# Performance work log

Hardware: AMD Instinct MI355X
Metric: run time of the kernel (lower is better)

## Reference

```python
import jax, jax.numpy as jnp
import numpy as np

B, NW, NS, SL = 32, 500, 50, 40
EMB, HID, VOCAB, E = 300, 150, 50000, 563200
N = B * (NW + NS)
MAXPOS = 512


def _sinusoid(n_pos, d):
    pos = np.arange(n_pos)[:, None].astype(np.float64)
    i = np.arange(d)[None, :]
    ang = pos / np.power(10000.0, 2 * (i // 2) / d)
    tab = np.zeros((n_pos, d))
    tab[:, 0::2] = np.sin(ang[:, 0::2])
    tab[:, 1::2] = np.cos(ang[:, 1::2])
    tab[0] = 0.0  # padding_idx=0
    return jnp.asarray(tab, dtype=jnp.float32)

_POS_TAB = _sinusoid(MAXPOS + 1, EMB)


def setup_inputs():
    keys = iter(jax.random.split(jax.random.key(0), 48))
    def nrm(shape, s=0.05):
        return jax.random.normal(next(keys), shape, dtype=jnp.float32) * s
    inp = {}
    inp["x"] = jax.random.randint(next(keys), (B, NW), 0, VOCAB, dtype=jnp.int32)
    inp["sent_x"] = jax.random.randint(next(keys), (B, NS, SL), 0, VOCAB, dtype=jnp.int32)
    inp["edge_index"] = jax.random.randint(next(keys), (2, E), 0, N, dtype=jnp.int32)
    inp["embed_table"] = nrm((VOCAB, EMB)).at[0].set(0.0)  # padding_idx=0
    for h in range(2, 8):
        inp["conv_w%d" % h] = nrm((50, 1, h, EMB))
        inp["conv_b%d" % h] = nrm((50,))
    inp["cnn_proj_w"] = nrm((HID, EMB)); inp["cnn_proj_b"] = nrm((HID,))
    inp["lstm_w_ih_l0"] = nrm((2, 4 * HID, HID)); inp["lstm_w_hh_l0"] = nrm((2, 4 * HID, HID))
    inp["lstm_b_ih_l0"] = nrm((2, 4 * HID)); inp["lstm_b_hh_l0"] = nrm((2, 4 * HID))
    inp["lstm_w_ih_l1"] = nrm((2, 4 * HID, 2 * HID)); inp["lstm_w_hh_l1"] = nrm((2, 4 * HID, HID))
    inp["lstm_b_ih_l1"] = nrm((2, 4 * HID)); inp["lstm_b_hh_l1"] = nrm((2, 4 * HID))
    inp["lstm_proj_w"] = nrm((HID, 2 * HID)); inp["lstm_proj_b"] = nrm((HID,))
    inp["gc0_w"] = nrm((HID, EMB)); inp["gc0_b"] = nrm((HID,))
    inp["gc1_w"] = nrm((HID, HID)); inp["gc1_b"] = nrm((HID,))
    inp["gc2_w"] = nrm((HID, HID)); inp["gc2_b"] = nrm((HID,))
    return inp


def _forward(x, sent_x, edge_index, embed_table, conv_ws, conv_bs,
             cnn_proj_w, cnn_proj_b, w_ih0, w_hh0, b_ih0, b_hh0,
             w_ih1, w_hh1, b_ih1, b_hh1, lstm_proj_w, lstm_proj_b,
             gc0_w, gc0_b, gc1_w, gc1_b, gc2_w, gc2_b):
    Bsz, S, L = sent_x.shape
    Nn = Bsz * S
    emb_words = embed_table[x]                                   # [B, NW, EMB]
    tok = embed_table[sent_x].reshape(Nn, L, EMB)                # [Nn, L, EMB]
    sentlen = (sent_x != 0).sum(-1).reshape(Nn)                  # token count per sentence
    a = jnp.arange(L)
    input_pos = jnp.where(a[None, :] < sentlen[:, None], a[None, :] + 1, 0)
    enc = tok + _POS_TAB[input_pos]
    # CNN ngram features: conv heights 2..7, full-width kernels == windowed matmuls
    feats = []
    for w, b in zip(conv_ws, conv_bs):
        h = w.shape[2]
        acc = b + sum(jnp.einsum('nld,od->nlo', enc[:, k:L - h + 1 + k, :], w[:, 0, k, :]) for k in range(h))
        feats.append(jnp.max(jax.nn.relu(acc), axis=1))          # [Nn, 50]
    ngram = jnp.concatenate(feats, axis=1)                        # [Nn, 300]
    snode_pos = jnp.tile(jnp.arange(S), Bsz)
    cnn_feat = ((ngram + _POS_TAB[snode_pos]) @ cnn_proj_w.T + cnn_proj_b).reshape(Bsz, S, HID)
    glen = (sent_x[:, :, 0] != 0).sum(-1)                         # valid sentence count per graph

    def lstm_dir(xs, w_ih, w_hh, bias):
        def step(carry, xt):
            hh, cc = carry
            g = xt @ w_ih.T + hh @ w_hh.T + bias
            i, f, gg, o = jnp.split(g, 4, axis=-1)
            cc = jax.nn.sigmoid(f) * cc + jax.nn.sigmoid(i) * jnp.tanh(gg)
            hh = jax.nn.sigmoid(o) * jnp.tanh(cc)
            return (hh, cc), hh
        z = jnp.zeros((xs.shape[0], HID), xs.dtype)
        _, hs = jax.lax.scan(step, (z, z), jnp.swapaxes(xs, 0, 1))
        return jnp.swapaxes(hs, 0, 1)

    def rev_within(xs):
        # reverse only the first glen[b] steps (packed-sequence semantics)
        T = xs.shape[1]; t = jnp.arange(T)
        idx = jnp.where(t[None, :] < glen[:, None], glen[:, None] - 1 - t[None, :], t[None, :])
        return jnp.take_along_axis(xs, idx[:, :, None], axis=1)

    def bidir(xs, w_ih, w_hh, b_i, b_h):
        f = lstm_dir(xs, w_ih[0], w_hh[0], b_i[0] + b_h[0])
        r = rev_within(lstm_dir(rev_within(xs), w_ih[1], w_hh[1], b_i[1] + b_h[1]))
        return jnp.concatenate([f, r], axis=-1)

    h1 = bidir(cnn_feat, w_ih0, w_hh0, b_ih0, b_hh0)
    h2 = bidir(h1, w_ih1, w_hh1, b_ih1, b_hh1)
    mask = (jnp.arange(S)[None, :] < glen[:, None]).astype(h2.dtype)[:, :, None]
    lstm_feat = (h2 * mask) @ lstm_proj_w.T + lstm_proj_b
    sent_out = jnp.concatenate([cnn_feat, lstm_feat], axis=-1)    # [B, S, 300]
    nodes = jnp.concatenate([emb_words, sent_out], axis=1)        # [B, NW+S, 300]
    nodes = (nodes @ gc0_w.T + gc0_b).reshape(-1, HID)            # [N, 150]
    Nt = nodes.shape[0]
    loop = jnp.arange(Nt, dtype=edge_index.dtype)
    src = jnp.concatenate([edge_index[0], loop])                  # add self-loops
    dst = jnp.concatenate([edge_index[1], loop])
    deg = jax.ops.segment_sum(jnp.ones(src.shape[0], nodes.dtype), dst, num_segments=Nt)
    dis = jnp.where(deg > 0, jax.lax.rsqrt(deg), 0.0)
    norm = (dis[src] * dis[dst])[:, None]

    def gcn(xin, w, bias):
        xw = xin @ w.T
        return jax.ops.segment_sum(xw[src] * norm, dst, num_segments=Nt) + bias

    h = jax.nn.elu(gcn(nodes, gc1_w, gc1_b))
    # F.dropout with training=False -> identity
    return gcn(h, gc2_w, gc2_b), emb_words


def reference(x, sent_x, edge_index, embed_table, conv_w2, conv_b2, conv_w3, conv_b3,
              conv_w4, conv_b4, conv_w5, conv_b5, conv_w6, conv_b6, conv_w7, conv_b7,
              cnn_proj_w, cnn_proj_b, lstm_w_ih_l0, lstm_w_hh_l0, lstm_b_ih_l0, lstm_b_hh_l0,
              lstm_w_ih_l1, lstm_w_hh_l1, lstm_b_ih_l1, lstm_b_hh_l1, lstm_proj_w, lstm_proj_b,
              gc0_w, gc0_b, gc1_w, gc1_b, gc2_w, gc2_b):
    conv_ws = [conv_w2, conv_w3, conv_w4, conv_w5, conv_w6, conv_w7]
    conv_bs = [conv_b2, conv_b3, conv_b4, conv_b5, conv_b6, conv_b7]
    return _forward(x, sent_x, edge_index, embed_table, conv_ws, conv_bs,
                    cnn_proj_w, cnn_proj_b, lstm_w_ih_l0, lstm_w_hh_l0, lstm_b_ih_l0, lstm_b_hh_l0,
                    lstm_w_ih_l1, lstm_w_hh_l1, lstm_b_ih_l1, lstm_b_hh_l1, lstm_proj_w, lstm_proj_b,
                    gc0_w, gc0_b, gc1_w, gc1_b, gc2_w, gc2_b)
```

## Files before the change

### kernel.cpp

```cpp
#include <hip/hip_runtime.h>
#include <stdint.h>
#include <math.h>

#define EDGES 563200
#define NNODES 17600
#define OUT0SZ 2640000
#define MROWS 64000
#define MPAD  64016
#define KSTRIDE 2112

typedef _Float16 h2 __attribute__((ext_vector_type(2)));
typedef _Float16 h4 __attribute__((ext_vector_type(4)));
typedef _Float16 v8h __attribute__((ext_vector_type(8)));
typedef float v4f __attribute__((ext_vector_type(4)));

__device__ __forceinline__ float sigm(float x){ return 1.f / (1.f + expf(-x)); }

__device__ __forceinline__ float fdot2_(h2 a, h2 b, float c){
#if __has_builtin(__builtin_amdgcn_fdot2)
  return __builtin_amdgcn_fdot2(a, b, c, false);
#else
  return c + (float)a.x * (float)b.x + (float)a.y * (float)b.y;
#endif
}

__device__ __forceinline__ void stage16(const char* g, char* lds_base, int lane){
#if __has_builtin(__builtin_amdgcn_global_load_lds)
  __builtin_amdgcn_global_load_lds(
      (const __attribute__((address_space(1))) void*)g,
      (__attribute__((address_space(3))) void*)lds_base, 16, 0, 0);
#else
  uint4 v = *(const uint4*)g;
  *(uint4*)(lds_base + lane * 16) = v;
#endif
}

__global__ void gcnk_postab(float* __restrict__ pos){
  int idx = blockIdx.x * 256 + threadIdx.x;
  if (idx >= 513 * 300) return;
  int p = idx / 300, i = idx - p * 300;
  float v = 0.f;
  if (p != 0){
    double expo = (double)(2 * (i / 2)) / 300.0;
    double ang = (double)p / pow(10000.0, expo);
    v = (float)((i & 1) ? cos(ang) : sin(ang));
  }
  pos[idx] = v;
}

__global__ void gcnk_prep(const int* __restrict__ sx, int* __restrict__ sentlen,
                          int* __restrict__ glen){
  int tid = blockIdx.x * 256 + threadIdx.x;
  if (tid < 1600){
    int c = 0;
    for (int j = 0; j < 40; j++) c += (sx[tid * 40 + j] != 0);
    sentlen[tid] = c;
  } else if (tid < 1632){
    int b = tid - 1600, c = 0;
    for (int s = 0; s < 50; s++) c += (sx[b * 2000 + s * 40] != 0);
    glen[b] = c;
  }
}

__global__ void gcnk_rowmap(const int* __restrict__ glen, int* __restrict__ rowmap){
  int i = blockIdx.x * 256 + threadIdx.x;
  if (i >= 1600) return;
  int b = i / 50, t = i - b * 50, g = glen[b];
  rowmap[i] = b * 50 + ((t < g) ? (g - 1 - t) : t);
}

__global__ void gcnk_embw(const int* __restrict__ x, const float* __restrict__ tab,
                          float4* __restrict__ out){
  int idx = blockIdx.x * 256 + threadIdx.x;
  if (idx >= 16000 * 75) return;
  int row = idx / 75, q = idx - row * 75;
  const float4* t = (const float4*)tab;
  out[idx] = t[x[row] * 75 + q];
}

__global__ void gcnk_zeroi(unsigned int* __restrict__ p, int n){
  int i = blockIdx.x * 256 + threadIdx.x;
  if (i < n) p[i] = 0u;
}

__global__ void gcnk_ench(const int* __restrict__ sx, const float* __restrict__ tab,
                          const float* __restrict__ pos, const int* __restrict__ sentlen,
                          _Float16* __restrict__ ench){
  int idx = blockIdx.x * 256 + threadIdx.x;
  if (idx >= MPAD * 75) return;
  int row = idx / 75, q = idx - row * 75;
  int d = q * 4;
  h4 o; o[0] = (_Float16)0.f; o[1] = (_Float16)0.f; o[2] = (_Float16)0.f; o[3] = (_Float16)0.f;
  if (row < MROWS){
    int n = row / 40, l = row - n * 40;
    int tok = sx[n * 40 + l];
    int p = (l < sentlen[n]) ? (l + 1) : 0;
    float4 a = *(const float4*)(tab + (size_t)tok * 300 + d);
    float4 b = *(const float4*)(pos + (size_t)p * 300 + d);
    o[0] = (_Float16)(a.x + b.x); o[1] = (_Float16)(a.y + b.y);
    o[2] = (_Float16)(a.z + b.z); o[3] = (_Float16)(a.w + b.w);
  }
  *(h4*)(ench + (size_t)row * 300 + d) = o;
}

__global__ void gcnk_bpack(const float* w2, const float* w3, const float* w4,
                           const float* w5, const float* w6, const float* w7,
                           const float* c2, const float* c3, const float* c4,
                           const float* c5, const float* c6, const float* c7,
                           _Float16* __restrict__ Bp, float* __restrict__ bias_p){
  int idx = blockIdx.x * 256 + threadIdx.x;
  if (idx < 2 * 160 * KSTRIDE){
    int n = idx / KSTRIDE, kk = idx - n * KSTRIDE;
    int g = n / 160, c = n - g * 160;
    _Float16 v = (_Float16)0.f;
    if (c < 150){
      int H = 3 * g + 2 + c / 50, o = c % 50;
      if (kk < 300 * H){
        const float* w;
        switch (H){ case 2: w = w2; break; case 3: w = w3; break;
                    case 4: w = w4; break; case 5: w = w5; break;
                    case 6: w = w6; break; default: w = w7; break; }
        v = (_Float16)w[o * 300 * H + kk];
      }
    }
    Bp[idx] = v;
  }
  if (idx < 320){
    int g = idx / 160, c = idx - g * 160;
    float bv = 0.f;
    if (c < 150){
      int H = 3 * g + 2 + c / 50, o = c % 50;
      const float* cbp;
      switch (H){ case 2: cbp = c2; break; case 3: cbp = c3; break;
                  case 4: cbp = c4; break; case 5: cbp = c5; break;
                  case 6: cbp = c6; break; default: cbp = c7; break; }
      bv = cbp[o];
    }
    bias_p[idx] = bv;
  }
}

__global__ __launch_bounds__(256)
void gcnk_convmfma(const _Float16* __restrict__ A, const _Float16* __restrict__ Bp,
                   const float* __restrict__ bias_p, unsigned int* __restrict__ ngram_u){
  __shared__ __align__(1024) char smem[36864];
  _Float16* Asm = (_Float16*)smem;
  _Float16* Bsm = (_Float16*)(smem + 16384);
  float* Cs = (float*)smem;
  const int tid = threadIdx.x;
  const int m0 = blockIdx.x * 128;
  const int grp = blockIdx.y;
  const char* Abase = (const char*)A;
  const char* Bbase = (const char*)(Bp + (size_t)grp * 160 * KSTRIDE);
  const int kmax = grp ? 2112 : 1216;
  const int w = tid >> 6, lane = tid & 63;
  const int wm = (w >> 1) * 64, wn = (w & 1) * 80;
  const int fm = lane & 15, fq = lane >> 4;
  const int lrow = lane >> 3;
  const int loff = (((lane & 7) ^ lrow) << 4);

  v4f acc[4][5] = {};

  for (int kc = 0; kc < kmax; kc += 64){
    #pragma unroll
    for (int ii = 0; ii < 4; ii++){
      int i = w * 4 + ii;
      const char* g = Abase + (size_t)(m0 + i * 8 + lrow) * 600 + kc * 2 + loff;
      stage16(g, (char*)Asm + i * 1024, lane);
    }
    #pragma unroll
    for (int jj = 0; jj < 5; jj++){
      int j = w * 5 + jj;
      const char* g = Bbase + (size_t)(j * 8 + lrow) * (KSTRIDE * 2) + kc * 2 + loff;
      stage16(g, (char*)Bsm + j * 1024, lane);
    }
    __syncthreads();
    #pragma unroll
    for (int ks = 0; ks < 2; ks++){
      const int axor = (ks * 64 + fq * 16) ^ ((fm & 7) << 4);
      v8h af[4], bf[5];
      #pragma unroll
      for (int mt = 0; mt < 4; mt++)
        af[mt] = *(const v8h*)((const char*)Asm + (wm + mt * 16 + fm) * 128 + axor);
      #pragma unroll
      for (int nt = 0; nt < 5; nt++)
        bf[nt] = *(const v8h*)((const char*)Bsm + (wn + nt * 16 + fm) * 128 + axor);
      #pragma unroll
      for (int mt = 0; mt < 4; mt++)
        #pragma unroll
        for (int nt = 0; nt < 5; nt++)
          acc[mt][nt] = __builtin_amdgcn_mfma_f32_16x16x32_f16(af[mt], bf[nt], acc[mt][nt], 0, 0, 0);
    }
    __syncthreads();
  }

  for (int p = 0; p < 5; p++){
    __syncthreads();
    #pragma unroll
    for (int nt = 0; nt < 5; nt++){
      int cstart = wn + nt * 16;
      if ((cstart >> 5) == p){
        int co = cstart - p * 32 + fm;
        #pragma unroll
        for (int mt = 0; mt < 4; mt++)
          #pragma unroll
          for (int r = 0; r < 4; r++)
            Cs[(wm + mt * 16 + fq * 4 + r) * 33 + co] = acc[mt][nt][r];
      }
    }
    __syncthreads();
    if (tid < 128){
      int cl = tid & 31, si = tid >> 5;
      int col = p * 32 + cl;
      if (col < 150){
        int H = 3 * grp + 2 + col / 50, lh = 41 - H;
        int sent = m0 / 40 + si;
        if (sent < 1600){
          int rlo = sent * 40; if (rlo < m0) rlo = m0;
          int rhi = sent * 40 + lh; if (rhi > m0 + 128) rhi = m0 + 128;
          if (rlo < rhi){
            float bv = bias_p[grp * 160 + col];
            float vmax = 0.f;
            for (int r = rlo; r < rhi; r++){
              float v = Cs[(r - m0) * 33 + cl] + bv;
              vmax = fmaxf(vmax, v);
            }
            atomicMax(ngram_u + sent * 300 + grp * 150 + col, __float_as_uint(vmax));
          }
        }
      }
    }
  }
}

__global__ void gcnk_addpos(float* __restrict__ ngram, const float* __restrict__ pos){
  int idx = blockIdx.x * 256 + threadIdx.x;
  if (idx >= 1600 * 300) return;
  int row = idx / 300, d = idx - row * 300;
  ngram[idx] += pos[(row % 50) * 300 + d];
}

template<int BM, int BN, int WMT, int WNT, int OUTH>
__global__ __launch_bounds__(256)
void gcnk_mgemm(const float* __restrict__ A, const float* __restrict__ Wt,
                const float* __restrict__ b1, const float* __restrict__ b2,
                void* __restrict__ Cv, int M, int N, int K){
  __shared__ __align__(16) _Float16 As[BM * 40];
  __shared__ __align__(16) _Float16 Bs[BN * 40];
  const int tid = threadIdx.x;
  const int m0 = blockIdx.x * BM, n0 = blockIdx.y * BN;
  const int w = tid >> 6, lane = tid & 63;
  const int wm = (w >> 1) * (WMT * 16), wn = (w & 1) * (WNT * 16);
  const int fm = lane & 15, fq = lane >> 4;
  v4f acc[WMT][WNT] = {};
  const int nch = (K + 31) >> 5;
  for (int ch = 0; ch < nch; ch++){
    int kc = ch * 32;
    #pragma unroll
    for (int j = 0; j < BM / 64; j++){
      int u = tid + 256 * j;
      int row = u >> 2, cb = (u & 3) * 8;
      int gm = m0 + row, gk = kc + cb;
      v8h vv;
      if (gm < M && gk + 8 <= K){
        const float* p = A + (size_t)gm * K + gk;
        #pragma unroll
        for (int e = 0; e < 8; e++) vv[e] = (_Float16)p[e];
      } else {
        #pragma unroll
        for (int e = 0; e < 8; e++)
          vv[e] = (gm < M && gk + e < K) ? (_Float16)A[(size_t)gm * K + gk + e] : (_Float16)0.f;
      }
      *(v8h*)(As + row * 40 + cb) = vv;
    }
    {
      int row = tid >> 2, cb = (tid & 3) * 8;
      int gn = n0 + row, gk = kc + cb;
      v8h vv;
      if (gn < N && gk + 8 <= K){
        const float* p = Wt + (size_t)gn * K + gk;
        #pragma unroll
        for (int e = 0; e < 8; e++) vv[e] = (_Float16)p[e];
      } else {
        #pragma unroll
        for (int e = 0; e < 8; e++)
          vv[e] = (gn < N && gk + e < K) ? (_Float16)Wt[(size_t)gn * K + gk + e] : (_Float16)0.f;
      }
      *(v8h*)(Bs + row * 40 + cb) = vv;
    }
    __syncthreads();
    v8h af[WMT], bf[WNT];
    #pragma unroll
    for (int mt = 0; mt < WMT; mt++)
      af[mt] = *(const v8h*)(As + (wm + mt * 16 + fm) * 40 + fq * 8);
    #pragma unroll
    for (int nt = 0; nt < WNT; nt++)
      bf[nt] = *(const v8h*)(Bs + (wn + nt * 16 + fm) * 40 + fq * 8);
    #pragma unroll
    for (int mt = 0; mt < WMT; mt++)
      #pragma unroll
      for (int nt = 0; nt < WNT; nt++)
        acc[mt][nt] = __builtin_amdgcn_mfma_f32_16x16x32_f16(af[mt], bf[nt], acc[mt][nt], 0, 0, 0);
    __syncthreads();
  }
  #pragma unroll
  for (int nt = 0; nt < WNT; nt++){
    int gn = n0 + wn + nt * 16 + fm;
    if (gn >= N) continue;
    float badd = (b1 ? b1[gn] : 0.f) + (b2 ? b2[gn] : 0.f);
    #pragma unroll
    for (int mt = 0; mt < WMT; mt++)
      #pragma unroll
      for (int r = 0; r < 4; r++){
        int gm = m0 + wm + mt * 16 + fq * 4 + r;
        if (gm < M){
          float val = acc[mt][nt][r] + badd;
          if (OUTH) ((_Float16*)Cv)[(size_t)gm * 160 + gn] = (_Float16)val;
          else      ((float*)Cv)[(size_t)gm * N + gn] = val;
        }
      }
  }
}

__global__ __launch_bounds__(256)
void gcnk_mgemmF(const float* __restrict__ A1, const int* __restrict__ mapA,
                 const float* __restrict__ A2, const int* __restrict__ mapB,
                 const int* __restrict__ glen, int usemask,
                 const float* __restrict__ Wt, const float* __restrict__ b1,
                 const float* __restrict__ b2, float* __restrict__ C,
                 int M, int N, int K){
  const int BM = 64, WMT = 2, WNT = 2;
  __shared__ __align__(16) _Float16 As[BM * 40];
  __shared__ __align__(16) _Float16 Bs[64 * 40];
  const int tid = threadIdx.x;
  const int m0 = blockIdx.x * BM, n0 = blockIdx.y * 64;
  const int w = tid >> 6, lane = tid & 63;
  const int wm = (w >> 1) * (WMT * 16), wn = (w & 1) * (WNT * 16);
  const int fm = lane & 15, fq = lane >> 4;
  v4f acc[WMT][WNT] = {};
  const int nch = (K + 31) >> 5;
  for (int ch = 0; ch < nch; ch++){
    int kc = ch * 32;
    {
      int row = tid >> 2, cb = (tid & 3) * 8;
      int gm = m0 + row, gk = kc + cb;
      v8h vv;
      bool ok = (gm < M);
      if (ok && usemask){
        int b = gm / 50;
        if (gm - b * 50 >= glen[b]) ok = false;
      }
      if (!ok){
        #pragma unroll
        for (int e = 0; e < 8; e++) vv[e] = (_Float16)0.f;
      } else if (!A2){
        int r = mapA ? mapA[gm] : gm;
        const float* base = A1 + (size_t)r * K;
        if (gk + 8 <= K){
          #pragma unroll
          for (int e = 0; e < 8; e++) vv[e] = (_Float16)base[gk + e];
        } else {
          #pragma unroll
          for (int e = 0; e < 8; e++)
            vv[e] = (gk + e < K) ? (_Float16)base[gk + e] : (_Float16)0.f;
        }
      } else {
        int rA = mapA ? mapA[gm] : gm;
        int rB = mapB ? mapB[gm] : gm;
        const float* pa = A1 + (size_t)rA * 150;
        const float* pb = A2 + (size_t)rB * 150;
        if (gk + 8 <= 150){
          #pragma unroll
          for (int e = 0; e < 8; e++) vv[e] = (_Float16)pa[gk + e];
        } else if (gk >= 150){
          #pragma unroll
          for (int e = 0; e < 8; e++)
            vv[e] = (gk + e < K) ? (_Float16)pb[gk + e - 150] : (_Float16)0.f;
        } else {
          #pragma unroll
          for (int e = 0; e < 8; e++){
            int c = gk + e;
            vv[e] = (c < 150) ? (_Float16)pa[c]
                  : ((c < K) ? (_Float16)pb[c - 150] : (_Float16)0.f);
          }
        }
      }
      *(v8h*)(As + row * 40 + cb) = vv;
    }
    {
      int row = tid >> 2, cb = (tid & 3) * 8;
      int gn = n0 + row, gk = kc + cb;
      v8h vv;
      if (gn < N && gk + 8 <= K){
        const float* p = Wt + (size_t)gn * K + gk;
        #pragma unroll
        for (int e = 0; e < 8; e++) vv[e] = (_Float16)p[e];
      } else {
        #pragma unroll
        for (int e = 0; e < 8; e++)
          vv[e] = (gn < N && gk + e < K) ? (_Float16)Wt[(size_t)gn * K + gk + e] : (_Float16)0.f;
      }
      *(v8h*)(Bs + row * 40 + cb) = vv;
    }
    __syncthreads();
    v8h af[WMT], bf[WNT];
    #pragma unroll
    for (int mt = 0; mt < WMT; mt++)
      af[mt] = *(const v8h*)(As + (wm + mt * 16 + fm) * 40 + fq * 8);
    #pragma unroll
    for (int nt = 0; nt < WNT; nt++)
      bf[nt] = *(const v8h*)(Bs + (wn + nt * 16 + fm) * 40 + fq * 8);
    #pragma unroll
    for (int mt = 0; mt < WMT; mt++)
      #pragma unroll
      for (int nt = 0; nt < WNT; nt++)
        acc[mt][nt] = __builtin_amdgcn_mfma_f32_16x16x32_f16(af[mt], bf[nt], acc[mt][nt], 0, 0, 0);
    __syncthreads();
  }
  #pragma unroll
  for (int nt = 0; nt < WNT; nt++){
    int gn = n0 + wn + nt * 16 + fm;
    if (gn >= N) continue;
    float badd = (b1 ? b1[gn] : 0.f) + (b2 ? b2[gn] : 0.f);
    #pragma unroll
    for (int mt = 0; mt < WMT; mt++)
      #pragma unroll
      for (int r = 0; r < 4; r++){
        int gm = m0 + wm + mt * 16 + fq * 4 + r;
        if (gm < M) C[(size_t)gm * N + gn] = acc[mt][nt][r] + badd;
      }
  }
}

__global__ __launch_bounds__(256)
void gcnk_mgemmN(const int* __restrict__ x, const float* __restrict__ tab,
                 const float* __restrict__ cnnf, const float* __restrict__ lstmf,
                 const float* __restrict__ Wt, const float* __restrict__ b1,
                 float* __restrict__ C, int N){
  const int M = NNODES, K = 300;
  __shared__ __align__(16) _Float16 As[128 * 40];
  __shared__ __align__(16) _Float16 Bs[64 * 40];
  const int tid = threadIdx.x;
  const int m0 = blockIdx.x * 128, n0 = blockIdx.y * 64;
  const int w = tid >> 6, lane = tid & 63;
  const int wm = (w >> 1) * 64, wn = (w & 1) * 32;
  const int fm = lane & 15, fq = lane >> 4;
  v4f acc[4][2] = {};
  for (int ch = 0; ch < 10; ch++){
    int kc = ch * 32;
    #pragma unroll
    for (int j = 0; j < 2; j++){
      int u = tid + 256 * j;
      int row = u >> 2, cb = (u & 3) * 8;
      int gm = m0 + row, gk = kc + cb;
      v8h vv;
      if (gm < M){
        int b = gm / 550, jj = gm - b * 550;
        if (jj < 500){
          const float* p = tab + (size_t)x[b * 500 + jj] * 300;
          if (gk + 8 <= 300){
            #pragma unroll
            for (int e = 0; e < 8; e++) vv[e] = (_Float16)p[gk + e];
          } else {
            #pragma unroll
            for (int e = 0; e < 8; e++)
              vv[e] = (gk + e < 300) ? (_Float16)p[gk + e] : (_Float16)0.f;
          }
        } else {
          int r = b * 50 + (jj - 500);
          const float* pa = cnnf + (size_t)r * 150;
          const float* pb = lstmf + (size_t)r * 150;
          if (gk + 8 <= 150){
            #pragma unroll
            for (int e = 0; e < 8; e++) vv[e] = (_Float16)pa[gk + e];
          } else if (gk >= 150 && gk + 8 <= 300){
            #pragma unroll
            for (int e = 0; e < 8; e++) vv[e] = (_Float16)pb[gk + e - 150];
          } else {
            #pragma unroll
            for (int e = 0; e < 8; e++){
              int c = gk + e;
              vv[e] = (c < 150) ? (_Float16)pa[c]
                    : ((c < 300) ? (_Float16)pb[c - 150] : (_Float16)0.f);
            }
          }
        }
      } else {
        #pragma unroll
        for (int e = 0; e < 8; e++) vv[e] = (_Float16)0.f;
      }
      *(v8h*)(As + row * 40 + cb) = vv;
    }
    {
      int row = tid >> 2, cb = (tid & 3) * 8;
      int gn = n0 + row, gk = kc + cb;
      v8h vv;
      if (gn < N && gk + 8 <= K){
        const float* p = Wt + (size_t)gn * K + gk;
        #pragma unroll
        for (int e = 0; e < 8; e++) vv[e] = (_Float16)p[e];
      } else {
        #pragma unroll
        for (int e = 0; e < 8; e++)
          vv[e] = (gn < N && gk + e < K) ? (_Float16)Wt[(size_t)gn * K + gk + e] : (_Float16)0.f;
      }
      *(v8h*)(Bs + row * 40 + cb) = vv;
    }
    __syncthreads();
    v8h af[4], bf[2];
    #pragma unroll
    for (int mt = 0; mt < 4; mt++)
      af[mt] = *(const v8h*)(As + (wm + mt * 16 + fm) * 40 + fq * 8);
    #pragma unroll
    for (int nt = 0; nt < 2; nt++)
      bf[nt] = *(const v8h*)(Bs + (wn + nt * 16 + fm) * 40 + fq * 8);
    #pragma unroll
    for (int mt = 0; mt < 4; mt++)
      #pragma unroll
      for (int nt = 0; nt < 2; nt++)
        acc[mt][nt] = __builtin_amdgcn_mfma_f32_16x16x32_f16(af[mt], bf[nt], acc[mt][nt], 0, 0, 0);
    __syncthreads();
  }
  #pragma unroll
  for (int nt = 0; nt < 2; nt++){
    int gn = n0 + wn + nt * 16 + fm;
    if (gn >= N) continue;
    float badd = b1[gn];
    #pragma unroll
    for (int mt = 0; mt < 4; mt++)
      #pragma unroll
      for (int r = 0; r < 4; r++){
        int gm = m0 + wm + mt * 16 + fq * 4 + r;
        if (gm < M) C[(size_t)gm * N + gn] = acc[mt][nt][r] + badd;
      }
  }
}

__global__ void gcnk_whhpack(const float* __restrict__ whh, _Float16* __restrict__ wpad){
  int idx = blockIdx.x * 256 + threadIdx.x;
  if (idx >= 1200 * 152) return;
  int row = idx / 152, col = idx - row * 152;
  wpad[idx] = (col < 150) ? (_Float16)whh[row * 150 + col] : (_Float16)0.f;
}

__global__ __launch_bounds__(640)
void gcnk_lstm(const float* __restrict__ xf, const float* __restrict__ xr,
               const _Float16* __restrict__ wpad, float* __restrict__ fo,
               float* __restrict__ ro){
  int b = blockIdx.x >> 1, dir = blockIdx.x & 1;
  const float* xih = dir ? xr : xf;
  float* out = dir ? ro : fo;
  __shared__ __align__(16) _Float16 hh[160];
  __shared__ float gates[600];
  const int tid = threadIdx.x;

  h2 w[76];
  if (tid < 600){
    const h2* wrow = (const h2*)(wpad + ((size_t)dir * 600 + tid) * 152);
    #pragma unroll
    for (int j = 0; j < 76; j++) w[j] = wrow[j];
  }
  for (int u = tid; u < 160; u += 640) hh[u] = (_Float16)0.f;
  float creg = 0.f;
  __syncthreads();

  for (int t = 0; t < 50; t++){
    if (tid < 600){
      float acc = xih[(b * 50 + t) * 600 + tid];
      float a0 = 0.f, a1 = 0.f, a2 = 0.f, a3 = 0.f;
      #pragma unroll
      for (int j = 0; j < 19; j++){
        union { float4 f; h2 h[4]; } u;
        u.f = *(const float4*)(hh + j * 8);
        a0 = fdot2_(w[4 * j + 0], u.h[0], a0);
        a1 = fdot2_(w[4 * j + 1], u.h[1], a1);
        a2 = fdot2_(w[4 * j + 2], u.h[2], a2);
        a3 = fdot2_(w[4 * j + 3], u.h[3], a3);
      }
      gates[tid] = acc + ((a0 + a1) + (a2 + a3));
    }
    __syncthreads();
    if (tid < 150){
      float ig = sigm(gates[tid]);
      float fg = sigm(gates[150 + tid]);
      float gg = tanhf(gates[300 + tid]);
      float og = sigm(gates[450 + tid]);
      creg = fg * creg + ig * gg;
      float hn = og * tanhf(creg);
      hh[tid] = (_Float16)hn;
      out[(b * 50 + t) * 150 + tid] = hn;
    }
    __syncthreads();
  }
}

__global__ void gcnk_hist(const int* __restrict__ ei, int* __restrict__ ecnt){
  int e = blockIdx.x * 256 + threadIdx.x;
  if (e < EDGES) atomicAdd(&ecnt[ei[EDGES + e]], 1);
}

__global__ __launch_bounds__(1024)
void gcnk_scan(const int* __restrict__ ecnt, int* __restrict__ eoff,
               int* __restrict__ ecur){
  __shared__ int wsum[16];
  int tid = threadIdx.x;
  int base = tid * 18;
  int pre[18];
  int s = 0;
  #pragma unroll
  for (int i = 0; i < 18; i++){
    int idx = base + i;
    int c = (idx < NNODES) ? ecnt[idx] : 0;
    pre[i] = s; s += c;
  }
  int lane = tid & 63, wid = tid >> 6;
  int run = s;
  #pragma unroll
  for (int off = 1; off < 64; off <<= 1){
    int y = __shfl_up(run, off, 64);
    if (lane >= off) run += y;
  }
  if (lane == 63) wsum[wid] = run;
  __syncthreads();
  if (tid == 0){
    int a = 0;
    #pragma unroll
    for (int i = 0; i < 16; i++){ int t2 = wsum[i]; wsum[i] = a; a += t2; }
  }
  __syncthreads();
  int excl = wsum[wid] + run - s;
  #pragma unroll
  for (int i = 0; i < 18; i++){
    int idx = base + i;
    if (idx < NNODES){
      int e = excl + pre[i];
      eoff[idx] = e; ecur[idx] = e;
    }
  }
}

__global__ void gcnk_scatter(const int* __restrict__ ei, int* __restrict__ ecur,
                             int* __restrict__ esrc){
  int e = blockIdx.x * 256 + threadIdx.x;
  if (e < EDGES){
    int d = ei[EDGES + e];
    int p = atomicAdd(&ecur[d], 1);
    esrc[p] = ei[e];
  }
}

__global__ void gcnk_dis2(const int* __restrict__ ecnt, float* __restrict__ dis){
  int i = blockIdx.x * 256 + threadIdx.x;
  if (i < NNODES) dis[i] = rsqrtf((float)(ecnt[i] + 1));
}

__global__ __launch_bounds__(128)
void gcnk_aggcsr_h(const int* __restrict__ eoff, const int* __restrict__ ecnt,
                   const int* __restrict__ esrc, const float* __restrict__ dis,
                   const _Float16* __restrict__ xw, const float* __restrict__ bias,
                   float* __restrict__ out, int doelu){
  int d = blockIdx.x, t = threadIdx.x;
  float dd = dis[d];
  bool act = t < 75;
  float ax = 0.f, ay = 0.f;
  if (act){
    h2 v = *(const h2*)(xw + (size_t)d * 160 + 2 * t);
    ax = (float)v[0] * dd; ay = (float)v[1] * dd;
  }
  int beg = eoff[d], end = beg + ecnt[d];
  for (int j = beg; j < end; j++){
    int s = esrc[j];
    float ds_ = dis[s];
    if (act){
      h2 v = *(const h2*)(xw + (size_t)s * 160 + 2 * t);
      ax += (float)v[0] * ds_; ay += (float)v[1] * ds_;
    }
  }
  if (act){
    float o0 = ax * dd + bias[2 * t];
    float o1 = ay * dd + bias[2 * t + 1];
    if (doelu){
      o0 = (o0 > 0.f) ? o0 : expm1f(o0);
      o1 = (o1 > 0.f) ? o1 : expm1f(o1);
    }
    *(float2*)(out + (size_t)d * 150 + 2 * t) = make_float2(o0, o1);
  }
}

extern "C" void kernel_launch(void* const* d_in, const int* in_sizes, int n_in,
                              void* d_out, int out_size, void* d_ws, size_t ws_size,
                              hipStream_t stream){
  (void)in_sizes; (void)n_in; (void)out_size; (void)ws_size;

  char* wsb = (char*)d_ws;
  size_t off = 0;
  auto alloc = [&](size_t bytes) -> void* {
    void* p = wsb + off;
    off = (off + bytes + 255) & ~(size_t)255;
    return p;
  };
  float* pos_tab  = (float*)alloc(513 * 300 * 4);
  int*   sentlen  = (int*)alloc(1600 * 4);
  int*   glen     = (int*)alloc(32 * 4);
  int*   rowmap   = (int*)alloc(1600 * 4);
  float* ngram    = (float*)alloc(1600 * 300 * 4);
  float* cnn_feat = (float*)alloc(1600 * 150 * 4);
  float* xih_f    = (float*)alloc(1600 * 600 * 4);
  float* xih_r    = (float*)alloc(1600 * 600 * 4);
  float* f0       = (float*)alloc(1600 * 150 * 4);
  float* r0       = (float*)alloc(1600 * 150 * 4);
  float* f1       = (float*)alloc(1600 * 150 * 4);
  float* r1       = (float*)alloc(1600 * 150 * 4);
  float* lstm_ft  = (float*)alloc(1600 * 150 * 4);
  float* nodes    = (float*)alloc((size_t)NNODES * 150 * 4);
  float* dis      = (float*)alloc(NNODES * 4);
  _Float16* xwh   = (_Float16*)alloc((size_t)NNODES * 160 * 2);
  _Float16* ench  = (_Float16*)alloc((size_t)MPAD * 300 * 2);
  _Float16* Bp    = (_Float16*)alloc((size_t)2 * 160 * KSTRIDE * 2);
  float* bias_p   = (float*)alloc(320 * 4);
  _Float16* wpad0 = (_Float16*)alloc(1200 * 152 * 2);
  _Float16* wpad1 = (_Float16*)alloc(1200 * 152 * 2);
  int*   ecnt     = (int*)alloc(NNODES * 4);
  int*   eoff     = (int*)alloc(NNODES * 4);
  int*   ecur     = (int*)alloc(NNODES * 4);
  int*   esrc     = (int*)alloc(EDGES * 4);

  const int*   x   = (const int*)d_in[0];
  const int*   sx  = (const int*)d_in[1];
  const int*   ei  = (const int*)d_in[2];
  const float* tab = (const float*)d_in[3];
  const float *cw[6], *cb[6];
  for (int h = 0; h < 6; h++){ cw[h] = (const float*)d_in[4 + 2 * h]; cb[h] = (const float*)d_in[5 + 2 * h]; }
  const float* cnnw = (const float*)d_in[16]; const float* cnnb = (const float*)d_in[17];
  const float* wih0 = (const float*)d_in[18]; const float* whh0 = (const float*)d_in[19];
  const float* bih0 = (const float*)d_in[20]; const float* bhh0 = (const float*)d_in[21];
  const float* wih1 = (const float*)d_in[22]; const float* whh1 = (const float*)d_in[23];
  const float* bih1 = (const float*)d_in[24]; const float* bhh1 = (const float*)d_in[25];
  const float* lpw  = (const float*)d_in[26]; const float* lpb  = (const float*)d_in[27];
  const float* g0w  = (const float*)d_in[28]; const float* g0b  = (const float*)d_in[29];
  const float* g1w  = (const float*)d_in[30]; const float* g1b  = (const float*)d_in[31];
  const float* g2w  = (const float*)d_in[32]; const float* g2b  = (const float*)d_in[33];

  float* out0 = (float*)d_out;
  float4* out1 = (float4*)((float*)d_out + OUT0SZ);

  auto mgemmLH = [&](const float* A, const float* W, void* C, int M, int N, int K){
    dim3 g((M + 127) / 128, (N + 63) / 64);
    gcnk_mgemm<128, 64, 4, 2, 1><<<g, 256, 0, stream>>>(A, W, nullptr, nullptr, C, M, N, K);
  };
  auto mgemmF = [&](const float* A1, const int* mapA, const float* A2, const int* mapB,
                    const int* gl, int um, const float* W, const float* b1,
                    const float* b2, float* C, int N, int K){
    dim3 g(25, (N + 63) / 64);
    gcnk_mgemmF<<<g, 256, 0, stream>>>(A1, mapA, A2, mapB, gl, um, W, b1, b2, C, 1600, N, K);
  };

  gcnk_postab<<<602, 256, 0, stream>>>(pos_tab);
  gcnk_prep<<<7, 256, 0, stream>>>(sx, sentlen, glen);
  gcnk_rowmap<<<7, 256, 0, stream>>>(glen, rowmap);
  gcnk_embw<<<4688, 256, 0, stream>>>(x, tab, out1);

  gcnk_zeroi<<<1875, 256, 0, stream>>>((unsigned int*)ngram, 1600 * 300);
  gcnk_ench<<<(MPAD * 75 + 255) / 256, 256, 0, stream>>>(sx, tab, pos_tab, sentlen, ench);
  gcnk_bpack<<<(2 * 160 * KSTRIDE + 255) / 256, 256, 0, stream>>>(
      cw[0], cw[1], cw[2], cw[3], cw[4], cw[5],
      cb[0], cb[1], cb[2], cb[3], cb[4], cb[5], Bp, bias_p);
  gcnk_whhpack<<<713, 256, 0, stream>>>(whh0, wpad0);
  gcnk_whhpack<<<713, 256, 0, stream>>>(whh1, wpad1);
  {
    dim3 g(500, 2);
    gcnk_convmfma<<<g, 256, 0, stream>>>(ench, Bp, bias_p, (unsigned int*)ngram);
  }
  gcnk_addpos<<<1875, 256, 0, stream>>>(ngram, pos_tab);
  mgemmF(ngram, nullptr, nullptr, nullptr, nullptr, 0, cnnw, cnnb, nullptr, cnn_feat, 150, 300);

  mgemmF(cnn_feat, nullptr, nullptr, nullptr, nullptr, 0,
         wih0,             bih0,       bhh0,       xih_f, 600, 150);
  mgemmF(cnn_feat, rowmap,  nullptr, nullptr, nullptr, 0,
         wih0 + 600 * 150, bih0 + 600, bhh0 + 600, xih_r, 600, 150);
  gcnk_lstm<<<64, 640, 0, stream>>>(xih_f, xih_r, wpad0, f0, r0);

  mgemmF(f0, nullptr, r0, rowmap, nullptr, 0,
         wih1,             bih1,       bhh1,       xih_f, 600, 300);
  mgemmF(f0, rowmap, r0, nullptr, nullptr, 0,
         wih1 + 600 * 300, bih1 + 600, bhh1 + 600, xih_r, 600, 300);
  gcnk_lstm<<<64, 640, 0, stream>>>(xih_f, xih_r, wpad1, f1, r1);

  mgemmF(f1, nullptr, r1, rowmap, glen, 1, lpw, lpb, nullptr, lstm_ft, 150, 300);

  {
    dim3 g(138, 3);
    gcnk_mgemmN<<<g, 256, 0, stream>>>(x, tab, cnn_feat, lstm_ft, g0w, g0b, nodes, 150);
  }

  gcnk_zeroi<<<69, 256, 0, stream>>>((unsigned int*)ecnt, NNODES);
  gcnk_hist<<<2200, 256, 0, stream>>>(ei, ecnt);
  gcnk_scan<<<1, 1024, 0, stream>>>(ecnt, eoff, ecur);
  gcnk_scatter<<<2200, 256, 0, stream>>>(ei, ecur, esrc);
  gcnk_dis2<<<69, 256, 0, stream>>>(ecnt, dis);

  mgemmLH(nodes, g1w, xwh, NNODES, 150, 150);
  gcnk_aggcsr_h<<<NNODES, 128, 0, stream>>>(eoff, ecnt, esrc, dis, xwh, g1b, nodes, 1);

  mgemmLH(nodes, g2w, xwh, NNODES, 150, 150);
  gcnk_aggcsr_h<<<NNODES, 128, 0, stream>>>(eoff, ecnt, esrc, dis, xwh, g2b, out0, 0);
}
```

Measured before the change: 847.2 us.

## Fuse small prep kernels, fold pos-add into GEMM, vectorize GEMM loads

Merges the prep and rowmap kernels into one single-block kernel, folds the positional-encoding add into the A-loading of the CNN projection GEMM, and folds the degree-normalisation computation into the scan kernel, which removes several launches. GEMM tile loads switch from scalar to float2 reads. The fused gather+GEMM for node inputs is replaced by a separate gather kernel into a new buffer followed by the generic mgemm, which adds an extra ~21MB write/read round trip. The CSR aggregation loop is unrolled by two with dual accumulators to expose more memory-level parallelism.

```diff
diff --git a/kernel.cpp b/kernel.cpp
--- a/kernel.cpp
+++ b/kernel.cpp
@@ -48,25 +48,26 @@
   pos[idx] = v;
 }
 
-__global__ void gcnk_prep(const int* __restrict__ sx, int* __restrict__ sentlen,
-                          int* __restrict__ glen){
-  int tid = blockIdx.x * 256 + threadIdx.x;
-  if (tid < 1600){
+__global__ __launch_bounds__(1024)
+void gcnk_prep2(const int* __restrict__ sx, int* __restrict__ sentlen,
+                int* __restrict__ glen_g, int* __restrict__ rowmap){
+  __shared__ int sg[32];
+  int tid = threadIdx.x;
+  for (int i = tid; i < 1600; i += 1024){
     int c = 0;
-    for (int j = 0; j < 40; j++) c += (sx[tid * 40 + j] != 0);
-    sentlen[tid] = c;
-  } else if (tid < 1632){
-    int b = tid - 1600, c = 0;
-    for (int s = 0; s < 50; s++) c += (sx[b * 2000 + s * 40] != 0);
-    glen[b] = c;
-  }
-}
-
-__global__ void gcnk_rowmap(const int* __restrict__ glen, int* __restrict__ rowmap){
-  int i = blockIdx.x * 256 + threadIdx.x;
-  if (i >= 1600) return;
-  int b = i / 50, t = i - b * 50, g = glen[b];
-  rowmap[i] = b * 50 + ((t < g) ? (g - 1 - t) : t);
+    for (int j = 0; j < 40; j++) c += (sx[i * 40 + j] != 0);
+    sentlen[i] = c;
+  }
+  if (tid < 32){
+    int c = 0;
+    for (int s = 0; s < 50; s++) c += (sx[tid * 2000 + s * 40] != 0);
+    glen_g[tid] = c; sg[tid] = c;
+  }
+  __syncthreads();
+  for (int i = tid; i < 1600; i += 1024){
+    int b = i / 50, t = i - b * 50, g = sg[b];
+    rowmap[i] = b * 50 + ((t < g) ? (g - 1 - t) : t);
+  }
 }
 
 __global__ void gcnk_embw(const int* __restrict__ x, const float* __restrict__ tab,
@@ -233,13 +234,6 @@
   }
 }
 
-__global__ void gcnk_addpos(float* __restrict__ ngram, const float* __restrict__ pos){
-  int idx = blockIdx.x * 256 + threadIdx.x;
-  if (idx >= 1600 * 300) return;
-  int row = idx / 300, d = idx - row * 300;
-  ngram[idx] += pos[(row % 50) * 300 + d];
-}
-
 template<int BM, int BN, int WMT, int WNT, int OUTH>
 __global__ __launch_bounds__(256)
 void gcnk_mgemm(const float* __restrict__ A, const float* __restrict__ Wt,
@@ -263,9 +257,12 @@
       int gm = m0 + row, gk = kc + cb;
       v8h vv;
       if (gm < M && gk + 8 <= K){
-        const float* p = A + (size_t)gm * K + gk;
-        #pragma unroll
-        for (int e = 0; e < 8; e++) vv[e] = (_Float16)p[e];
+        const float2* p = (const float2*)(A + (size_t)gm * K + gk);
+        float2 q0 = p[0], q1 = p[1], q2 = p[2], q3 = p[3];
+        vv[0] = (_Float16)q0.x; vv[1] = (_Float16)q0.y;
+        vv[2] = (_Float16)q1.x; vv[3] = (_Float16)q1.y;
+        vv[4] = (_Float16)q2.x; vv[5] = (_Float16)q2.y;
+        vv[6] = (_Float16)q3.x; vv[7] = (_Float16)q3.y;
       } else {
         #pragma unroll
         for (int e = 0; e < 8; e++)
@@ -278,9 +275,12 @@
       int gn = n0 + row, gk = kc + cb;
       v8h vv;
       if (gn < N && gk + 8 <= K){
-        const float* p = Wt + (size_t)gn * K + gk;
-        #pragma unroll
-        for (int e = 0; e < 8; e++) vv[e] = (_Float16)p[e];
+        const float2* p = (const float2*)(Wt + (size_t)gn * K + gk);
+        float2 q0 = p[0], q1 = p[1], q2 = p[2], q3 = p[3];
+        vv[0] = (_Float16)q0.x; vv[1] = (_Float16)q0.y;
+        vv[2] = (_Float16)q1.x; vv[3] = (_Float16)q1.y;
+        vv[4] = (_Float16)q2.x; vv[5] = (_Float16)q2.y;
+        vv[6] = (_Float16)q3.x; vv[7] = (_Float16)q3.y;
       } else {
         #pragma unroll
         for (int e = 0; e < 8; e++)
@@ -326,6 +326,7 @@
 void gcnk_mgemmF(const float* __restrict__ A1, const int* __restrict__ mapA,
                  const float* __restrict__ A2, const int* __restrict__ mapB,
                  const int* __restrict__ glen, int usemask,
+                 const float* __restrict__ apos,
                  const float* __restrict__ Wt, const float* __restrict__ b1,
                  const float* __restrict__ b2, float* __restrict__ C,
                  int M, int N, int K){
@@ -357,12 +358,26 @@
         int r = mapA ? mapA[gm] : gm;
         const float* base = A1 + (size_t)r * K;
         if (gk + 8 <= K){
-          #pragma unroll
-          for (int e = 0; e < 8; e++) vv[e] = (_Float16)base[gk + e];
+          const float2* p = (const float2*)(base + gk);
+          float2 q0 = p[0], q1 = p[1], q2 = p[2], q3 = p[3];
+          if (apos){
+            const float2* a2 = (const float2*)(apos + (size_t)(gm % 50) * K + gk);
+            float2 r0 = a2[0], r1 = a2[1], r2 = a2[2], r3 = a2[3];
+            q0.x += r0.x; q0.y += r0.y; q1.x += r1.x; q1.y += r1.y;
+            q2.x += r2.x; q2.y += r2.y; q3.x += r3.x; q3.y += r3.y;
+          }
+          vv[0] = (_Float16)q0.x; vv[1] = (_Float16)q0.y;
+          vv[2] = (_Float16)q1.x; vv[3] = (_Float16)q1.y;
+          vv[4] = (_Float16)q2.x; vv[5] = (_Float16)q2.y;
+          vv[6] = (_Float16)q3.x; vv[7] = (_Float16)q3.y;
         } else {
           #pragma unroll
-          for (int e = 0; e < 8; e++)
-            vv[e] = (gk + e < K) ? (_Float16)base[gk + e] : (_Float16)0.f;
+          for (int e = 0; e < 8; e++){
+            int c = gk + e;
+            float vf = (c < K) ? base[c] : 0.f;
+            if (apos && c < K) vf += apos[(size_t)(gm % 50) * K + c];
+            vv[e] = (_Float16)vf;
+          }
         }
       } else {
         int rA = mapA ? mapA[gm] : gm;
@@ -370,12 +385,19 @@
         const float* pa = A1 + (size_t)rA * 150;
         const float* pb = A2 + (size_t)rB * 150;
         if (gk + 8 <= 150){
-          #pragma unroll
-          for (int e = 0; e < 8; e++) vv[e] = (_Float16)pa[gk + e];
-        } else if (gk >= 150){
-          #pragma unroll
-          for (int e = 0; e < 8; e++)
-            vv[e] = (gk + e < K) ? (_Float16)pb[gk + e - 150] : (_Float16)0.f;
+          const float2* p = (const float2*)(pa + gk);
+          float2 q0 = p[0], q1 = p[1], q2 = p[2], q3 = p[3];
+          vv[0] = (_Float16)q0.x; vv[1] = (_Float16)q0.y;
+          vv[2] = (_Float16)q1.x; vv[3] = (_Float16)q1.y;
+          vv[4] = (_Float16)q2.x; vv[5] = (_Float16)q2.y;
+          vv[6] = (_Float16)q3.x; vv[7] = (_Float16)q3.y;
+        } else if (gk >= 152 && gk + 8 <= K){
+          const float2* p = (const float2*)(pb + gk - 150);
+          float2 q0 = p[0], q1 = p[1], q2 = p[2], q3 = p[3];
+          vv[0] = (_Float16)q0.x; vv[1] = (_Float16)q0.y;
+          vv[2] = (_Float16)q1.x; vv[3] = (_Float16)q1.y;
+          vv[4] = (_Float16)q2.x; vv[5] = (_Float16)q2.y;
+          vv[6] = (_Float16)q3.x; vv[7] = (_Float16)q3.y;
         } else {
           #pragma unroll
           for (int e = 0; e < 8; e++){
@@ -392,9 +414,12 @@
       int gn = n0 + row, gk = kc + cb;
       v8h vv;
       if (gn < N && gk + 8 <= K){
-        const float* p = Wt + (size_t)gn * K + gk;
-        #pragma unroll
-        for (int e = 0; e < 8; e++) vv[e] = (_Float16)p[e];
+        const float2* p = (const float2*)(Wt + (size_t)gn * K + gk);
+        float2 q0 = p[0], q1 = p[1], q2 = p[2], q3 = p[3];
+        vv[0] = (_Float16)q0.x; vv[1] = (_Float16)q0.y;
+        vv[2] = (_Float16)q1.x; vv[3] = (_Float16)q1.y;
+        vv[4] = (_Float16)q2.x; vv[5] = (_Float16)q2.y;
+        vv[6] = (_Float16)q3.x; vv[7] = (_Float16)q3.y;
       } else {
         #pragma unroll
         for (int e = 0; e < 8; e++)
@@ -432,108 +457,20 @@
   }
 }
 
-__global__ __launch_bounds__(256)
-void gcnk_mgemmN(const int* __restrict__ x, const float* __restrict__ tab,
-                 const float* __restrict__ cnnf, const float* __restrict__ lstmf,
-                 const float* __restrict__ Wt, const float* __restrict__ b1,
-                 float* __restrict__ C, int N){
-  const int M = NNODES, K = 300;
-  __shared__ __align__(16) _Float16 As[128 * 40];
-  __shared__ __align__(16) _Float16 Bs[64 * 40];
-  const int tid = threadIdx.x;
-  const int m0 = blockIdx.x * 128, n0 = blockIdx.y * 64;
-  const int w = tid >> 6, lane = tid & 63;
-  const int wm = (w >> 1) * 64, wn = (w & 1) * 32;
-  const int fm = lane & 15, fq = lane >> 4;
-  v4f acc[4][2] = {};
-  for (int ch = 0; ch < 10; ch++){
-    int kc = ch * 32;
-    #pragma unroll
-    for (int j = 0; j < 2; j++){
-      int u = tid + 256 * j;
-      int row = u >> 2, cb = (u & 3) * 8;
-      int gm = m0 + row, gk = kc + cb;
-      v8h vv;
-      if (gm < M){
-        int b = gm / 550, jj = gm - b * 550;
-        if (jj < 500){
-          const float* p = tab + (size_t)x[b * 500 + jj] * 300;
-          if (gk + 8 <= 300){
-            #pragma unroll
-            for (int e = 0; e < 8; e++) vv[e] = (_Float16)p[gk + e];
-          } else {
-            #pragma unroll
-            for (int e = 0; e < 8; e++)
-              vv[e] = (gk + e < 300) ? (_Float16)p[gk + e] : (_Float16)0.f;
-          }
-        } else {
-          int r = b * 50 + (jj - 500);
-          const float* pa = cnnf + (size_t)r * 150;
-          const float* pb = lstmf + (size_t)r * 150;
-          if (gk + 8 <= 150){
-            #pragma unroll
-            for (int e = 0; e < 8; e++) vv[e] = (_Float16)pa[gk + e];
-          } else if (gk >= 150 && gk + 8 <= 300){
-            #pragma unroll
-            for (int e = 0; e < 8; e++) vv[e] = (_Float16)pb[gk + e - 150];
-          } else {
-            #pragma unroll
-            for (int e = 0; e < 8; e++){
-              int c = gk + e;
-              vv[e] = (c < 150) ? (_Float16)pa[c]
-                    : ((c < 300) ? (_Float16)pb[c - 150] : (_Float16)0.f);
-            }
-          }
-        }
-      } else {
-        #pragma unroll
-        for (int e = 0; e < 8; e++) vv[e] = (_Float16)0.f;
-      }
-      *(v8h*)(As + row * 40 + cb) = vv;
-    }
-    {
-      int row = tid >> 2, cb = (tid & 3) * 8;
-      int gn = n0 + row, gk = kc + cb;
-      v8h vv;
-      if (gn < N && gk + 8 <= K){
-        const float* p = Wt + (size_t)gn * K + gk;
-        #pragma unroll
-        for (int e = 0; e < 8; e++) vv[e] = (_Float16)p[e];
-      } else {
-        #pragma unroll
-        for (int e = 0; e < 8; e++)
-          vv[e] = (gn < N && gk + e < K) ? (_Float16)Wt[(size_t)gn * K + gk + e] : (_Float16)0.f;
-      }
-      *(v8h*)(Bs + row * 40 + cb) = vv;
-    }
-    __syncthreads();
-    v8h af[4], bf[2];
-    #pragma unroll
-    for (int mt = 0; mt < 4; mt++)
-      af[mt] = *(const v8h*)(As + (wm + mt * 16 + fm) * 40 + fq * 8);
-    #pragma unroll
-    for (int nt = 0; nt < 2; nt++)
-      bf[nt] = *(const v8h*)(Bs + (wn + nt * 16 + fm) * 40 + fq * 8);
-    #pragma unroll
-    for (int mt = 0; mt < 4; mt++)
-      #pragma unroll
-      for (int nt = 0; nt < 2; nt++)
-        acc[mt][nt] = __builtin_amdgcn_mfma_f32_16x16x32_f16(af[mt], bf[nt], acc[mt][nt], 0, 0, 0);
-    __syncthreads();
-  }
-  #pragma unroll
-  for (int nt = 0; nt < 2; nt++){
-    int gn = n0 + wn + nt * 16 + fm;
-    if (gn >= N) continue;
-    float badd = b1[gn];
-    #pragma unroll
-    for (int mt = 0; mt < 4; mt++)
-      #pragma unroll
-      for (int r = 0; r < 4; r++){
-        int gm = m0 + wm + mt * 16 + fq * 4 + r;
-        if (gm < M) C[(size_t)gm * N + gn] = acc[mt][nt][r] + badd;
-      }
-  }
+__global__ void gcnk_nodes_in(const int* __restrict__ x, const float* __restrict__ tab,
+                              const float* __restrict__ cnnf, const float* __restrict__ lstmf,
+                              float* __restrict__ out){
+  int idx = blockIdx.x * 256 + threadIdx.x;
+  if (idx >= NNODES * 300) return;
+  int nrow = idx / 300, d = idx - nrow * 300;
+  int b = nrow / 550, j = nrow - b * 550;
+  float v;
+  if (j < 500) v = tab[x[b * 500 + j] * 300 + d];
+  else {
+    int r = b * 50 + (j - 500);
+    v = (d < 150) ? cnnf[r * 150 + d] : lstmf[r * 150 + d - 150];
+  }
+  out[idx] = v;
 }
 
 __global__ void gcnk_whhpack(const float* __restrict__ whh, _Float16* __restrict__ wpad){
@@ -601,7 +538,7 @@
 
 __global__ __launch_bounds__(1024)
 void gcnk_scan(const int* __restrict__ ecnt, int* __restrict__ eoff,
-               int* __restrict__ ecur){
+               int* __restrict__ ecur, float* __restrict__ dis){
   __shared__ int wsum[16];
   int tid = threadIdx.x;
   int base = tid * 18;
@@ -611,6 +548,7 @@
   for (int i = 0; i < 18; i++){
     int idx = base + i;
     int c = (idx < NNODES) ? ecnt[idx] : 0;
+    if (idx < NNODES) dis[idx] = rsqrtf((float)(c + 1));
     pre[i] = s; s += c;
   }
   int lane = tid & 63, wid = tid >> 6;
@@ -649,11 +587,6 @@
   }
 }
 
-__global__ void gcnk_dis2(const int* __restrict__ ecnt, float* __restrict__ dis){
-  int i = blockIdx.x * 256 + threadIdx.x;
-  if (i < NNODES) dis[i] = rsqrtf((float)(ecnt[i] + 1));
-}
-
 __global__ __launch_bounds__(128)
 void gcnk_aggcsr_h(const int* __restrict__ eoff, const int* __restrict__ ecnt,
                    const int* __restrict__ esrc, const float* __restrict__ dis,
@@ -662,23 +595,34 @@
   int d = blockIdx.x, t = threadIdx.x;
   float dd = dis[d];
   bool act = t < 75;
-  float ax = 0.f, ay = 0.f;
+  float ax0 = 0.f, ay0 = 0.f, ax1 = 0.f, ay1 = 0.f;
   if (act){
     h2 v = *(const h2*)(xw + (size_t)d * 160 + 2 * t);
-    ax = (float)v[0] * dd; ay = (float)v[1] * dd;
+    ax0 = (float)v[0] * dd; ay0 = (float)v[1] * dd;
   }
   int beg = eoff[d], end = beg + ecnt[d];
-  for (int j = beg; j < end; j++){
+  int j = beg;
+  for (; j + 1 < end; j += 2){
+    int s0 = esrc[j], s1 = esrc[j + 1];
+    float d0 = dis[s0], d1 = dis[s1];
+    if (act){
+      h2 v0 = *(const h2*)(xw + (size_t)s0 * 160 + 2 * t);
+      h2 v1 = *(const h2*)(xw + (size_t)s1 * 160 + 2 * t);
+      ax0 += (float)v0[0] * d0; ay0 += (float)v0[1] * d0;
+      ax1 += (float)v1[0] * d1; ay1 += (float)v1[1] * d1;
+    }
+  }
+  if (j < end){
     int s = esrc[j];
     float ds_ = dis[s];
     if (act){
       h2 v = *(const h2*)(xw + (size_t)s * 160 + 2 * t);
-      ax += (float)v[0] * ds_; ay += (float)v[1] * ds_;
+      ax0 += (float)v[0] * ds_; ay0 += (float)v[1] * ds_;
     }
   }
   if (act){
-    float o0 = ax * dd + bias[2 * t];
-    float o1 = ay * dd + bias[2 * t + 1];
+    float o0 = (ax0 + ax1) * dd + bias[2 * t];
+    float o1 = (ay0 + ay1) * dd + bias[2 * t + 1];
     if (doelu){
       o0 = (o0 > 0.f) ? o0 : expm1f(o0);
       o1 = (o1 > 0.f) ? o1 : expm1f(o1);
@@ -712,6 +656,7 @@
   float* f1       = (float*)alloc(1600 * 150 * 4);
   float* r1       = (float*)alloc(1600 * 150 * 4);
   float* lstm_ft  = (float*)alloc(1600 * 150 * 4);
+  float* nodes_in = (float*)alloc((size_t)NNODES * 300 * 4);
   float* nodes    = (float*)alloc((size_t)NNODES * 150 * 4);
   float* dis      = (float*)alloc(NNODES * 4);
   _Float16* xwh   = (_Float16*)alloc((size_t)NNODES * 160 * 2);
@@ -744,20 +689,24 @@
   float* out0 = (float*)d_out;
   float4* out1 = (float4*)((float*)d_out + OUT0SZ);
 
+  auto mgemmL = [&](const float* A, const float* W, const float* b1, const float* b2,
+                    void* C, int M, int N, int K){
+    dim3 g((M + 127) / 128, (N + 63) / 64);
+    gcnk_mgemm<128, 64, 4, 2, 0><<<g, 256, 0, stream>>>(A, W, b1, b2, C, M, N, K);
+  };
   auto mgemmLH = [&](const float* A, const float* W, void* C, int M, int N, int K){
     dim3 g((M + 127) / 128, (N + 63) / 64);
     gcnk_mgemm<128, 64, 4, 2, 1><<<g, 256, 0, stream>>>(A, W, nullptr, nullptr, C, M, N, K);
   };
   auto mgemmF = [&](const float* A1, const int* mapA, const float* A2, const int* mapB,
-                    const int* gl, int um, const float* W, const float* b1,
-                    const float* b2, float* C, int N, int K){
+                    const int* gl, int um, const float* apos, const float* W,
+                    const float* b1, const float* b2, float* C, int N, int K){
     dim3 g(25, (N + 63) / 64);
-    gcnk_mgemmF<<<g, 256, 0, stream>>>(A1, mapA, A2, mapB, gl, um, W, b1, b2, C, 1600, N, K);
+    gcnk_mgemmF<<<g, 256, 0, stream>>>(A1, mapA, A2, mapB, gl, um, apos, W, b1, b2, C, 1600, N, K);
   };
 
   gcnk_postab<<<602, 256, 0, stream>>>(pos_tab);
-  gcnk_prep<<<7, 256, 0, stream>>>(sx, sentlen, glen);
-  gcnk_rowmap<<<7, 256, 0, stream>>>(glen, rowmap);
+  gcnk_prep2<<<1, 1024, 0, stream>>>(sx, sentlen, glen, rowmap);
   gcnk_embw<<<4688, 256, 0, stream>>>(x, tab, out1);
 
   gcnk_zeroi<<<1875, 256, 0, stream>>>((unsigned int*)ngram, 1600 * 300);
@@ -771,33 +720,30 @@
     dim3 g(500, 2);
     gcnk_convmfma<<<g, 256, 0, stream>>>(ench, Bp, bias_p, (unsigned int*)ngram);
   }
-  gcnk_addpos<<<1875, 256, 0, stream>>>(ngram, pos_tab);
-  mgemmF(ngram, nullptr, nullptr, nullptr, nullptr, 0, cnnw, cnnb, nullptr, cnn_feat, 150, 300);
-
-  mgemmF(cnn_feat, nullptr, nullptr, nullptr, nullptr, 0,
+  mgemmF(ngram, nullptr, nullptr, nullptr, nullptr, 0, pos_tab,
+         cnnw, cnnb, nullptr, cnn_feat, 150, 300);
+
+  mgemmF(cnn_feat, nullptr, nullptr, nullptr, nullptr, 0, nullptr,
          wih0,             bih0,       bhh0,       xih_f, 600, 150);
-  mgemmF(cnn_feat, rowmap,  nullptr, nullptr, nullptr, 0,
+  mgemmF(cnn_feat, rowmap,  nullptr, nullptr, nullptr, 0, nullptr,
          wih0 + 600 * 150, bih0 + 600, bhh0 + 600, xih_r, 600, 150);
   gcnk_lstm<<<64, 640, 0, stream>>>(xih_f, xih_r, wpad0, f0, r0);
 
-  mgemmF(f0, nullptr, r0, rowmap, nullptr, 0,
+  mgemmF(f0, nullptr, r0, rowmap, nullptr, 0, nullptr,
          wih1,             bih1,       bhh1,       xih_f, 600, 300);
-  mgemmF(f0, rowmap, r0, nullptr, nullptr, 0,
+  mgemmF(f0, rowmap, r0, nullptr, nullptr, 0, nullptr,
          wih1 + 600 * 300, bih1 + 600, bhh1 + 600, xih_r, 600, 300);
   gcnk_lstm<<<64, 640, 0, stream>>>(xih_f, xih_r, wpad1, f1, r1);
 
-  mgemmF(f1, nullptr, r1, rowmap, glen, 1, lpw, lpb, nullptr, lstm_ft, 150, 300);
-
-  {
-    dim3 g(138, 3);
-    gcnk_mgemmN<<<g, 256, 0, stream>>>(x, tab, cnn_feat, lstm_ft, g0w, g0b, nodes, 150);
-  }
+  mgemmF(f1, nullptr, r1, rowmap, glen, 1, nullptr, lpw, lpb, nullptr, lstm_ft, 150, 300);
+
+  gcnk_nodes_in<<<20625, 256, 0, stream>>>(x, tab, cnn_feat, lstm_ft, nodes_in);
+  mgemmL(nodes_in, g0w, g0b, nullptr, nodes, NNODES, 150, 300);
 
   gcnk_zeroi<<<69, 256, 0, stream>>>((unsigned int*)ecnt, NNODES);
   gcnk_hist<<<2200, 256, 0, stream>>>(ei, ecnt);
-  gcnk_scan<<<1, 1024, 0, stream>>>(ecnt, eoff, ecur);
+  gcnk_scan<<<1, 1024, 0, stream>>>(ecnt, eoff, ecur, dis);
   gcnk_scatter<<<2200, 256, 0, stream>>>(ei, ecur, esrc);
-  gcnk_dis2<<<69, 256, 0, stream>>>(ecnt, dis);
 
   mgemmLH(nodes, g1w, xwh, NNODES, 150, 150);
   gcnk_aggcsr_h<<<NNODES, 128, 0, stream>>>(eoff, ecnt, esrc, dis, xwh, g1b, nodes, 1);
```

Measured after the change: 811.0 us. 1.04x faster.
